# Kernel optimization log

Measured on AMD Instinct MI355X. Metric: run time of the kernel, lower is better.

The kernel has to match this reference:

```python
import jax, jax.numpy as jnp
import numpy as np
from jax import lax

B, C, H, W = 16, 128, 96, 96  # dim = C


def conv2d(x, w, b, pad, groups=1):
    y = lax.conv_general_dilated(
        x, w, window_strides=(1, 1), padding=[(pad, pad), (pad, pad)],
        dimension_numbers=("NCHW", "OIHW", "NCHW"), feature_group_count=groups)
    return y + b[None, :, None, None]


def setup_inputs() -> dict:
    key = jax.random.key(0)
    ks = jax.random.split(key, 16)
    std = 0.02
    inp = {
        "x": jax.random.normal(ks[0], (B, C, H, W), jnp.float32),
        "sin": jax.random.normal(ks[1], (H * W, C), jnp.float32),
        "cos": jax.random.normal(ks[2], (H * W, C), jnp.float32),
        # qkvo: 1x1 conv, dim -> 4*dim
        "w_qkvo": jax.random.normal(ks[3], (4 * C, C, 1, 1), jnp.float32) * std,
        "b_qkvo": jnp.zeros((4 * C,), jnp.float32),
        # lepe: 5x5 depthwise conv
        "w_lepe": jax.random.normal(ks[4], (C, 1, 5, 5), jnp.float32) * std,
        "b_lepe": jnp.zeros((C,), jnp.float32),
        # proj: 1x1 conv
        "w_proj": jax.random.normal(ks[5], (C, C, 1, 1), jnp.float32) * std,
        "b_proj": jnp.zeros((C,), jnp.float32),
        # 3x3 depthwise convs on q/k/v
        "w_q": jax.random.normal(ks[6], (C, 1, 3, 3), jnp.float32) * std,
        "b_q": jnp.zeros((C,), jnp.float32),
        "w_k": jax.random.normal(ks[7], (C, 1, 3, 3), jnp.float32) * std,
        "b_k": jnp.zeros((C,), jnp.float32),
        "w_v": jax.random.normal(ks[8], (C, 1, 3, 3), jnp.float32) * std,
        "b_v": jnp.zeros((C,), jnp.float32),
    }
    return inp


def reference(x, sin, cos, w_qkvo, b_qkvo, w_lepe, b_lepe, w_proj, b_proj,
              w_q, b_q, w_k, b_k, w_v, b_v):
    # sin/cos are accepted but unused, matching the original forward.
    b, c, h, w = x.shape
    hw = h * w
    scale = c ** (-0.5)

    qkvo = conv2d(x, w_qkvo, b_qkvo, 0)          # (B, 4C, H, W)
    qkv = qkvo[:, :3 * c]
    o = qkvo[:, 3 * c:]
    lepe = conv2d(qkv[:, 2 * c:], w_lepe, b_lepe, 2, groups=c)  # (B, C, H, W)

    q = qkv[:, :c]
    k = qkv[:, c:2 * c]
    v = qkv[:, 2 * c:]
    q = q + conv2d(q, w_q, b_q, 1, groups=c)
    k = k + conv2d(k, w_k, b_k, 1, groups=c)
    v = v + conv2d(v, w_v, b_v, 1, groups=c)

    # (B, C, H, W) -> (B, HW, C)
    to_tok = lambda t: t.reshape(b, c, hw).transpose(0, 2, 1)
    q = jax.nn.elu(to_tok(q)) + 1.0
    k = jax.nn.elu(to_tok(k)) + 1.0
    v = to_tok(v)

    k_mean = k.mean(axis=1, keepdims=True)                    # (B, 1, C)
    z = jnp.einsum("bnc,bmc->bnm", q, k_mean) * scale         # (B, HW, 1)

    s = (scale / hw) ** 0.5
    kv = jnp.einsum("bnc,bnd->bcd", k * s, v * s)             # (B, C, C)

    res = (jnp.einsum("bnc,bcd->bnd", q, kv) * (1.0 + 1.0 / (z + 1e-6))
           - z * v.mean(axis=2, keepdims=True))               # (B, HW, C)

    res = res.transpose(0, 2, 1).reshape(b, c, h, w)
    res = res + lepe
    return conv2d(res * o, w_proj, b_proj, 0)
```

## Files before the change

kernel.cpp:

```cpp
#include <hip/hip_runtime.h>
#include <math.h>

#define HW 9216
#define BSTRIDE_QKVO ((size_t)4718592)
#define BSTRIDE_C    ((size_t)1179648)
#define KVS 24

typedef __attribute__((ext_vector_type(4))) short short4v;
typedef __attribute__((ext_vector_type(8))) short short8v;
typedef __attribute__((ext_vector_type(4))) float f32x4;
typedef __attribute__((ext_vector_type(4))) unsigned short u16x4;

__device__ __forceinline__ unsigned short f2b(float f) {
  union { float f; unsigned u; } v; v.f = f;
  unsigned r = (v.u + 0x7fffu + ((v.u >> 16) & 1u)) >> 16;
  return (unsigned short)r;
}
__device__ __forceinline__ float b2f(unsigned short h) {
  union { unsigned u; float f; } v; v.u = ((unsigned)h) << 16;
  return v.f;
}

__global__ void cvt_kernel(const float* __restrict__ in, unsigned short* __restrict__ out, int n) {
  int i = blockIdx.x * 256 + threadIdx.x;
  if (i < n) out[i] = f2b(in[i]);
}

template<int BSRC_F32, int OUT_F32, int NOCB>
__global__ __launch_bounds__(256) void gemm_k128s(
    const unsigned short* __restrict__ A, const void* __restrict__ Bv,
    const float* __restrict__ bias, void* __restrict__ Ov,
    size_t bstrB, size_t bstrO)
{
  __shared__ unsigned short Bt[128 * 132];
  const int t = threadIdx.x, lane = t & 63, wave = t >> 6;
  const int wr = wave >> 1, wc = wave & 1;
  const int l4 = lane & 15, lg = lane >> 4;
  const int pb = blockIdx.x << 7, b = blockIdx.y;

  if (BSRC_F32) {
    const float* B = (const float*)Bv + (size_t)b * bstrB;
    #pragma unroll
    for (int i = 0; i < 8; ++i) {
      int id = t + (i << 8);
      int kp = id >> 5, pg = id & 31;
      const float* r0 = B + (size_t)(2 * kp) * HW + pb + (pg << 2);
      f32x4 a = *(const f32x4*)r0;
      f32x4 c = *(const f32x4*)(r0 + HW);
      #pragma unroll
      for (int j = 0; j < 4; ++j)
        *(unsigned*)&Bt[((pg << 2) + j) * 132 + 2 * kp] =
            (unsigned)f2b(a[j]) | ((unsigned)f2b(c[j]) << 16);
    }
  } else {
    const unsigned short* B = (const unsigned short*)Bv + (size_t)b * bstrB;
    #pragma unroll
    for (int i = 0; i < 8; ++i) {
      int id = t + (i << 8);
      int kp = id >> 5, pg = id & 31;
      const unsigned short* r0 = B + (size_t)(2 * kp) * HW + pb + (pg << 2);
      u16x4 a = *(const u16x4*)r0;
      u16x4 c = *(const u16x4*)(r0 + HW);
      #pragma unroll
      for (int j = 0; j < 4; ++j)
        *(unsigned*)&Bt[((pg << 2) + j) * 132 + 2 * kp] =
            (unsigned)a[j] | ((unsigned)c[j] << 16);
    }
  }

  __syncthreads();

  short8v af[4][4];
  #pragma unroll
  for (int mp = 0; mp < 4; ++mp)
    #pragma unroll
    for (int ks = 0; ks < 4; ++ks) {
      int base = (wr * 64 + mp * 16 + l4) * 132 + ks * 32 + lg * 8;
      short4v lo = *(const short4v*)&Bt[base];
      short4v hi = *(const short4v*)&Bt[base + 4];
      short8v v;
      v[0] = lo[0]; v[1] = lo[1]; v[2] = lo[2]; v[3] = lo[3];
      v[4] = hi[0]; v[5] = hi[1]; v[6] = hi[2]; v[7] = hi[3];
      af[mp][ks] = v;
    }

  for (int co = 0; co < NOCB; ++co) {
    f32x4 acc[4][4];
    #pragma unroll
    for (int mp = 0; mp < 4; ++mp)
      #pragma unroll
      for (int nd = 0; nd < 4; ++nd) acc[mp][nd] = (f32x4){0.f, 0.f, 0.f, 0.f};

    #pragma unroll
    for (int ks = 0; ks < 4; ++ks) {
      short8v bfk[4];
      #pragma unroll
      for (int nd = 0; nd < 4; ++nd)
        bfk[nd] = *(const short8v*)(A + (size_t)(co * 128 + wc * 64 + nd * 16 + l4) * 128 + ks * 32 + lg * 8);
      #pragma unroll
      for (int nd = 0; nd < 4; ++nd)
        #pragma unroll
        for (int mp = 0; mp < 4; ++mp)
          acc[mp][nd] = __builtin_amdgcn_mfma_f32_16x16x32_bf16(af[mp][ks], bfk[nd], acc[mp][nd], 0, 0, 0);
    }

    float bb[4];
    #pragma unroll
    for (int nd = 0; nd < 4; ++nd) bb[nd] = bias[co * 128 + wc * 64 + nd * 16 + l4];

    if (OUT_F32) {
      float* O = (float*)Ov + (size_t)b * bstrO;
      #pragma unroll
      for (int mp = 0; mp < 4; ++mp) {
        int px = pb + wr * 64 + mp * 16 + lg * 4;
        #pragma unroll
        for (int nd = 0; nd < 4; ++nd) {
          int oc = co * 128 + wc * 64 + nd * 16 + l4;
          f32x4 v;
          #pragma unroll
          for (int i = 0; i < 4; ++i) v[i] = acc[mp][nd][i] + bb[nd];
          *(f32x4*)&O[(size_t)oc * HW + px] = v;
        }
      }
    } else {
      unsigned short* O = (unsigned short*)Ov + (size_t)b * bstrO;
      #pragma unroll
      for (int mp = 0; mp < 4; ++mp) {
        int px = pb + wr * 64 + mp * 16 + lg * 4;
        #pragma unroll
        for (int nd = 0; nd < 4; ++nd) {
          int oc = co * 128 + wc * 64 + nd * 16 + l4;
          u16x4 v;
          #pragma unroll
          for (int i = 0; i < 4; ++i) v[i] = f2b(acc[mp][nd][i] + bb[nd]);
          *(u16x4*)&O[(size_t)oc * HW + px] = v;
        }
      }
    }
  }
}

__device__ __forceinline__ void stage_plane(const unsigned short* __restrict__ g,
                                            float* __restrict__ sp, int t) {
  #pragma unroll
  for (int i = 0; i < 9; ++i) {
    int f = (t + (i << 8)) << 2;
    u16x4 u = *(const u16x4*)&g[f];
    f32x4 fv;
    fv[0] = b2f(u[0]); fv[1] = b2f(u[1]); fv[2] = b2f(u[2]); fv[3] = b2f(u[3]);
    *(f32x4*)&sp[f] = fv;
  }
}

__device__ __forceinline__ f32x4 conv3_strip(const float* __restrict__ sp, int base,
                                             const float* __restrict__ w9,
                                             bool j0, bool j23, f32x4* cen) {
  f32x4 acc = (f32x4){0.f, 0.f, 0.f, 0.f};
  #pragma unroll
  for (int ky = 0; ky < 3; ++ky) {
    const float* rowp = sp + base + (ky - 1) * 96;
    f32x4 w0 = *(const f32x4*)(rowp - 4);
    f32x4 w1 = *(const f32x4*)(rowp);
    f32x4 w2 = *(const f32x4*)(rowp + 4);
    float xm1 = j0 ? 0.f : w0[3];
    float xp4 = j23 ? 0.f : w2[0];
    float k0 = w9[ky * 3], k1 = w9[ky * 3 + 1], k2 = w9[ky * 3 + 2];
    acc[0] += k0 * xm1   + k1 * w1[0] + k2 * w1[1];
    acc[1] += k0 * w1[0] + k1 * w1[1] + k2 * w1[2];
    acc[2] += k0 * w1[1] + k1 * w1[2] + k2 * w1[3];
    acc[3] += k0 * w1[2] + k1 * w1[3] + k2 * xp4;
    if (ky == 1) *cen = w1;
  }
  return acc;
}

__global__ __launch_bounds__(256) void dwconv_kernel(
    unsigned short* __restrict__ qkvo,
    const float* __restrict__ w_q, const float* __restrict__ b_q,
    const float* __restrict__ w_k, const float* __restrict__ b_k,
    const float* __restrict__ w_v, const float* __restrict__ b_v,
    const float* __restrict__ w_lepe, const float* __restrict__ b_lepe,
    float* __restrict__ lp, float* __restrict__ ksum)
{
  __shared__ float sb[9612];
  __shared__ float red[256];
  const int c = blockIdx.x, b = blockIdx.y, t = threadIdx.x;
  unsigned short* qg = qkvo + ((size_t)b * 512 + c) * HW;
  unsigned short* kg = qg + (size_t)128 * HW;
  unsigned short* vg = qg + (size_t)256 * HW;
  float* lg = lp + ((size_t)b * 128 + c) * HW;
  float* sp = sb + 196;

  for (int i = t; i < 384; i += 256) {
    int idx = (i < 192) ? (i - 192) : (9024 + i);
    sp[idx] = 0.f;
  }

  {
    stage_plane(qg, sp, t);
    float w9[9];
    #pragma unroll
    for (int i = 0; i < 9; ++i) w9[i] = w_q[c * 9 + i];
    float bb = b_q[c];
    __syncthreads();
    for (int i = 0; i < 9; ++i) {
      int s = t + (i << 8);
      int r = s / 24, j = s - r * 24;
      int base = r * 96 + (j << 2);
      f32x4 cen;
      f32x4 a = conv3_strip(sp, base, w9, j == 0, j == 23, &cen);
      u16x4 o;
      #pragma unroll
      for (int k = 0; k < 4; ++k) {
        float v = cen[k] + bb + a[k];
        o[k] = f2b(v > 0.f ? v + 1.f : __expf(v));
      }
      *(u16x4*)&qg[base] = o;
    }
    __syncthreads();
  }
  float kacc = 0.f;
  {
    stage_plane(kg, sp, t);
    float w9[9];
    #pragma unroll
    for (int i = 0; i < 9; ++i) w9[i] = w_k[c * 9 + i];
    float bb = b_k[c];
    __syncthreads();
    for (int i = 0; i < 9; ++i) {
      int s = t + (i << 8);
      int r = s / 24, j = s - r * 24;
      int base = r * 96 + (j << 2);
      f32x4 cen;
      f32x4 a = conv3_strip(sp, base, w9, j == 0, j == 23, &cen);
      u16x4 o;
      #pragma unroll
      for (int k = 0; k < 4; ++k) {
        float v = cen[k] + bb + a[k];
        float e = v > 0.f ? v + 1.f : __expf(v);
        o[k] = f2b(e);
        kacc += e;
      }
      *(u16x4*)&kg[base] = o;
    }
    __syncthreads();
  }
  {
    stage_plane(vg, sp, t);
    float w9[9], w25[25];
    #pragma unroll
    for (int i = 0; i < 9; ++i) w9[i] = w_v[c * 9 + i];
    #pragma unroll
    for (int i = 0; i < 25; ++i) w25[i] = w_lepe[c * 25 + i];
    float bv = b_v[c], bl = b_lepe[c];
    __syncthreads();
    for (int i = 0; i < 9; ++i) {
      int s = t + (i << 8);
      int r = s / 24, j = s - r * 24;
      int base = r * 96 + (j << 2);
      bool j0 = (j == 0), j23 = (j == 23);
      f32x4 a3 = (f32x4){0.f, 0.f, 0.f, 0.f};
      f32x4 a5 = (f32x4){0.f, 0.f, 0.f, 0.f};
      f32x4 cen = (f32x4){0.f, 0.f, 0.f, 0.f};
      #pragma unroll
      for (int ky = 0; ky < 5; ++ky) {
        const float* rowp = sp + base + (ky - 2) * 96;
        f32x4 w0 = *(const f32x4*)(rowp - 4);
        f32x4 w1 = *(const f32x4*)(rowp);
        f32x4 w2 = *(const f32x4*)(rowp + 4);
        float xm2 = j0 ? 0.f : w0[2];
        float xm1 = j0 ? 0.f : w0[3];
        float xp4 = j23 ? 0.f : w2[0];
        float xp5 = j23 ? 0.f : w2[1];
        const float* wr5 = w25 + ky * 5;
        a5[0] += wr5[0]*xm2   + wr5[1]*xm1   + wr5[2]*w1[0] + wr5[3]*w1[1] + wr5[4]*w1[2];
        a5[1] += wr5[0]*xm1   + wr5[1]*w1[0] + wr5[2]*w1[1] + wr5[3]*w1[2] + wr5[4]*w1[3];
        a5[2] += wr5[0]*w1[0] + wr5[1]*w1[1] + wr5[2]*w1[2] + wr5[3]*w1[3] + wr5[4]*xp4;
        a5[3] += wr5[0]*w1[1] + wr5[1]*w1[2] + wr5[2]*w1[3] + wr5[3]*xp4   + wr5[4]*xp5;
        if (ky >= 1 && ky <= 3) {
          float k0 = w9[(ky-1)*3], k1 = w9[(ky-1)*3+1], k2 = w9[(ky-1)*3+2];
          a3[0] += k0 * xm1   + k1 * w1[0] + k2 * w1[1];
          a3[1] += k0 * w1[0] + k1 * w1[1] + k2 * w1[2];
          a3[2] += k0 * w1[1] + k1 * w1[2] + k2 * w1[3];
          a3[3] += k0 * w1[2] + k1 * w1[3] + k2 * xp4;
          if (ky == 2) cen = w1;
        }
      }
      u16x4 o;
      f32x4 lout;
      #pragma unroll
      for (int k = 0; k < 4; ++k) {
        o[k] = f2b(cen[k] + bv + a3[k]);
        lout[k] = bl + a5[k];
      }
      *(u16x4*)&vg[base] = o;
      *(f32x4*)&lg[base] = lout;
    }
  }
  red[t] = kacc; __syncthreads();
  for (int s2 = 128; s2 > 0; s2 >>= 1) { if (t < s2) red[t] += red[t + s2]; __syncthreads(); }
  if (t == 0) ksum[b * 128 + c] = red[0];
}

__global__ __launch_bounds__(256) void kv_mfma(
    const unsigned short* __restrict__ qkvo, float* __restrict__ part)
{
  const int t = threadIdx.x, lane = t & 63, wave = t >> 6;
  const int wr = wave >> 1, wc = wave & 1;
  const int l4 = lane & 15, lg = lane >> 4;
  const int s = blockIdx.x, b = blockIdx.y;
  const unsigned short* kbase = qkvo + (size_t)b * BSTRIDE_QKVO + (size_t)128 * HW;
  const unsigned short* vbase = kbase + (size_t)128 * HW;
  const int p0 = s * 384;

  f32x4 acc[4][4];
  #pragma unroll
  for (int m = 0; m < 4; ++m)
    #pragma unroll
    for (int n = 0; n < 4; ++n) acc[m][n] = (f32x4){0.f, 0.f, 0.f, 0.f};

  for (int kk = 0; kk < 12; ++kk) {
    int p = p0 + kk * 32 + lg * 8;
    short8v ka[4], va[4];
    #pragma unroll
    for (int m = 0; m < 4; ++m) ka[m] = *(const short8v*)(kbase + (size_t)(wr * 64 + m * 16 + l4) * HW + p);
    #pragma unroll
    for (int n = 0; n < 4; ++n) va[n] = *(const short8v*)(vbase + (size_t)(wc * 64 + n * 16 + l4) * HW + p);
    #pragma unroll
    for (int n = 0; n < 4; ++n)
      #pragma unroll
      for (int m = 0; m < 4; ++m)
        acc[m][n] = __builtin_amdgcn_mfma_f32_16x16x32_bf16(ka[m], va[n], acc[m][n], 0, 0, 0);
  }

  float* pp = part + ((size_t)b * KVS + s) * 16384;
  #pragma unroll
  for (int m = 0; m < 4; ++m)
    #pragma unroll
    for (int n = 0; n < 4; ++n) {
      int d = wc * 64 + n * 16 + l4;
      #pragma unroll
      for (int i = 0; i < 4; ++i) {
        int cch = wr * 64 + m * 16 + lg * 4 + i;
        pp[(cch << 7) + d] = acc[m][n][i];
      }
    }
}

__global__ void kvreduce(const float* __restrict__ part, unsigned short* __restrict__ kvT) {
  const int b = blockIdx.y;
  const int e0 = blockIdx.x * 2048 + threadIdx.x;
  const float* pb_ = part + (size_t)b * KVS * 16384;
  for (int i = 0; i < 8; ++i) {
    int e = e0 + i * 256;
    int cch = e >> 7, d = e & 127;
    float sum = 0.f;
    #pragma unroll 8
    for (int s = 0; s < KVS; ++s) sum += pb_[(size_t)s * 16384 + e];
    kvT[(size_t)b * 16384 + d * 128 + cch] = f2b(sum);
  }
}

__global__ void vmean_k(const unsigned short* __restrict__ qkvo, float* __restrict__ vmean) {
  const int b = blockIdx.y;
  const int px = blockIdx.x * 256 + threadIdx.x;
  const unsigned short* vb = qkvo + (size_t)b * BSTRIDE_QKVO + (size_t)256 * HW + px;
  float s = 0.f;
  #pragma unroll 8
  for (int d = 0; d < 128; ++d) s += b2f(vb[(size_t)d * HW]);
  vmean[(size_t)b * HW + px] = s * (1.f / 128.f);
}

__global__ __launch_bounds__(256) void attn_mfma(
    unsigned short* __restrict__ qkvo, const unsigned short* __restrict__ kvT,
    const float* __restrict__ ksum, const float* __restrict__ vmean,
    const float* __restrict__ lp)
{
  __shared__ unsigned short Bt[128 * 132];
  __shared__ float zb[128];
  __shared__ float km[128];
  const int t = threadIdx.x, lane = t & 63, wave = t >> 6;
  const int wr = wave >> 1, wc = wave & 1;
  const int l4 = lane & 15, lg = lane >> 4;
  const int pb = blockIdx.x << 7, b = blockIdx.y;
  const float kSCf = (float)(0.08838834764831843 / 9216.0);

  unsigned short* qs = qkvo + (size_t)b * BSTRIDE_QKVO;
  const unsigned short* os = qs + (size_t)384 * HW;
  const float* lpb = lp + (size_t)b * BSTRIDE_C;

  if (t < 128) km[t] = ksum[(b << 7) + t];

  #pragma unroll
  for (int i = 0; i < 8; ++i) {
    int id = t + (i << 8);
    int kp = id >> 5, pg = id & 31;
    const unsigned short* r0 = qs + (size_t)(2 * kp) * HW + pb + (pg << 2);
    u16x4 a = *(const u16x4*)r0;
    u16x4 c = *(const u16x4*)(r0 + HW);
    #pragma unroll
    for (int j = 0; j < 4; ++j)
      *(unsigned*)&Bt[((pg << 2) + j) * 132 + 2 * kp] =
          (unsigned)a[j] | ((unsigned)c[j] << 16);
  }

  const unsigned short* Ab = kvT + (size_t)b * 16384;
  short8v bkv[4][4];
  #pragma unroll
  for (int nd = 0; nd < 4; ++nd)
    #pragma unroll
    for (int ks = 0; ks < 4; ++ks)
      bkv[nd][ks] = *(const short8v*)(Ab + (size_t)(wc * 64 + nd * 16 + l4) * 128 + ks * 32 + lg * 8);

  f32x4 acc[4][4];
  #pragma unroll
  for (int mp = 0; mp < 4; ++mp)
    #pragma unroll
    for (int nd = 0; nd < 4; ++nd) acc[mp][nd] = (f32x4){0.f, 0.f, 0.f, 0.f};

  __syncthreads();

  if (t < 128) {
    float za = 0.f;
    #pragma unroll 8
    for (int cch = 0; cch < 128; ++cch) za += b2f(Bt[t * 132 + cch]) * km[cch];
    zb[t] = za;
  }

  #pragma unroll
  for (int ks = 0; ks < 4; ++ks) {
    short8v aq[4];
    #pragma unroll
    for (int mp = 0; mp < 4; ++mp) {
      int base = (wr * 64 + mp * 16 + l4) * 132 + ks * 32 + lg * 8;
      short4v lo = *(const short4v*)&Bt[base];
      short4v hi = *(const short4v*)&Bt[base + 4];
      short8v v;
      v[0] = lo[0]; v[1] = lo[1]; v[2] = lo[2]; v[3] = lo[3];
      v[4] = hi[0]; v[5] = hi[1]; v[6] = hi[2]; v[7] = hi[3];
      aq[mp] = v;
    }
    #pragma unroll
    for (int nd = 0; nd < 4; ++nd)
      #pragma unroll
      for (int mp = 0; mp < 4; ++mp)
        acc[mp][nd] = __builtin_amdgcn_mfma_f32_16x16x32_bf16(aq[mp], bkv[nd][ks], acc[mp][nd], 0, 0, 0);
  }

  __syncthreads();

  #pragma unroll
  for (int mp = 0; mp < 4; ++mp) {
    int pxl = wr * 64 + mp * 16 + lg * 4;
    int px = pb + pxl;
    f32x4 zv = *(const f32x4*)&zb[pxl];
    f32x4 vm = *(const f32x4*)&vmean[(size_t)b * HW + px];
    f32x4 zfv, zvmv;
    #pragma unroll
    for (int i = 0; i < 4; ++i) {
      float z = zv[i] * kSCf;
      zfv[i]  = kSCf * (1.f + 1.f / (z + 1e-6f));
      zvmv[i] = z * vm[i];
    }
    #pragma unroll
    for (int nd = 0; nd < 4; ++nd) {
      int d = wc * 64 + nd * 16 + l4;
      f32x4 le = *(const f32x4*)&lpb[(size_t)d * HW + px];
      u16x4 ovv = *(const u16x4*)&os[(size_t)d * HW + px];
      u16x4 o;
      #pragma unroll
      for (int i = 0; i < 4; ++i) {
        float r = (acc[mp][nd][i] * zfv[i] - zvmv[i] + le[i]) * b2f(ovv[i]);
        o[i] = f2b(r);
      }
      *(u16x4*)&qs[(size_t)d * HW + px] = o;
    }
  }
}

extern "C" void kernel_launch(void* const* d_in, const int* in_sizes, int n_in,
                              void* d_out, int out_size, void* d_ws, size_t ws_size,
                              hipStream_t stream) {
  const float* x      = (const float*)d_in[0];
  const float* w_qkvo = (const float*)d_in[3];
  const float* b_qkvo = (const float*)d_in[4];
  const float* w_lepe = (const float*)d_in[5];
  const float* b_lepe = (const float*)d_in[6];
  const float* w_proj = (const float*)d_in[7];
  const float* b_proj = (const float*)d_in[8];
  const float* w_q = (const float*)d_in[9];
  const float* b_q = (const float*)d_in[10];
  const float* w_k = (const float*)d_in[11];
  const float* b_k = (const float*)d_in[12];
  const float* w_v = (const float*)d_in[13];
  const float* b_v = (const float*)d_in[14];
  float* out = (float*)d_out;

  unsigned short* wqh = (unsigned short*)d_ws;
  unsigned short* wph = wqh + 65536;
  const size_t perb_bytes = 9437184 + 1572864 + 32768 + 512 + 36864;
  int G = 0;
  for (int g = 16; g >= 1; g >>= 1)
    if ((size_t)163840 + (size_t)g * perb_bytes <= ws_size) { G = g; break; }
  if (G == 0) return;

  size_t off = 163840;
  unsigned short* qkvo_h = (unsigned short*)((char*)d_ws + off); off += (size_t)G * 9437184;
  float* kvpart = (float*)((char*)d_ws + off);                   off += (size_t)G * 1572864;
  unsigned short* kvT = (unsigned short*)((char*)d_ws + off);    off += (size_t)G * 32768;
  float* ksum = (float*)((char*)d_ws + off);                     off += (size_t)G * 512;
  float* vmeanp = (float*)((char*)d_ws + off);

  cvt_kernel<<<dim3(256), 256, 0, stream>>>(w_qkvo, wqh, 65536);
  cvt_kernel<<<dim3(64),  256, 0, stream>>>(w_proj, wph, 16384);

  for (int b0 = 0; b0 < 16; b0 += G) {
    const float* xc  = x   + (size_t)b0 * BSTRIDE_C;
    float*       oc_ = out + (size_t)b0 * BSTRIDE_C;

    gemm_k128s<1, 0, 4><<<dim3(72, G), 256, 0, stream>>>(
        wqh, xc, b_qkvo, qkvo_h, BSTRIDE_C, BSTRIDE_QKVO);
    dwconv_kernel<<<dim3(128, G), 256, 0, stream>>>(qkvo_h, w_q, b_q, w_k, b_k, w_v, b_v,
                                                    w_lepe, b_lepe, oc_, ksum);
    kv_mfma<<<dim3(KVS, G), 256, 0, stream>>>(qkvo_h, kvpart);
    kvreduce<<<dim3(8, G), 256, 0, stream>>>(kvpart, kvT);
    vmean_k<<<dim3(36, G), 256, 0, stream>>>(qkvo_h, vmeanp);
    attn_mfma<<<dim3(72, G), 256, 0, stream>>>(qkvo_h, kvT, ksum, vmeanp, oc_);
    gemm_k128s<0, 1, 1><<<dim3(72, G), 256, 0, stream>>>(
        wph, qkvo_h, b_proj, oc_, BSTRIDE_QKVO, BSTRIDE_C);
  }
}
```

Before: 299.4 us.

## Double-buffer GEMM input tiles across three 64-pixel tiles per block

Both 1x1-conv GEMMs now have each block handle three 64-pixel tiles instead of one 128-pixel tile. A two-slot LDS buffer lets the global loads for the next tile run while the MFMA compute for the current tile proceeds. The grid drops from 72 to 48 blocks per batch, and launch bounds now request 3 blocks per CU to keep occupancy up despite the register-held prefetch. The risks are fewer blocks for the GPU to spread across, and smaller per-wave tiles that lower MFMA reuse of the weight fragments loaded from global memory.

```diff
diff --git a/kernel.cpp b/kernel.cpp
--- a/kernel.cpp
+++ b/kernel.cpp
@@ -27,116 +27,150 @@
 }
 
 template<int BSRC_F32, int OUT_F32, int NOCB>
-__global__ __launch_bounds__(256) void gemm_k128s(
+__global__ __launch_bounds__(256, 3) void gemm_pipe(
     const unsigned short* __restrict__ A, const void* __restrict__ Bv,
     const float* __restrict__ bias, void* __restrict__ Ov,
     size_t bstrB, size_t bstrO)
 {
-  __shared__ unsigned short Bt[128 * 132];
+  __shared__ unsigned short Bt[2][64 * 132];
   const int t = threadIdx.x, lane = t & 63, wave = t >> 6;
   const int wr = wave >> 1, wc = wave & 1;
   const int l4 = lane & 15, lg = lane >> 4;
-  const int pb = blockIdx.x << 7, b = blockIdx.y;
-
-  if (BSRC_F32) {
-    const float* B = (const float*)Bv + (size_t)b * bstrB;
-    #pragma unroll
-    for (int i = 0; i < 8; ++i) {
+  const int b = blockIdx.y;
+
+  f32x4 ra[4], rc[4];
+  u16x4 ha[4], hc[4];
+
+  const float* Bf = (const float*)Bv + (size_t)b * bstrB;
+  const unsigned short* Bh = (const unsigned short*)Bv + (size_t)b * bstrB;
+
+  auto stage_load = [&](int tile) {
+    int pb = tile << 6;
+    if (BSRC_F32) {
+      #pragma unroll
+      for (int i = 0; i < 4; ++i) {
+        int id = t + (i << 8);
+        int kp = id >> 4, pg = id & 15;
+        const float* r0 = Bf + (size_t)(2 * kp) * HW + pb + (pg << 2);
+        ra[i] = *(const f32x4*)r0;
+        rc[i] = *(const f32x4*)(r0 + HW);
+      }
+    } else {
+      #pragma unroll
+      for (int i = 0; i < 4; ++i) {
+        int id = t + (i << 8);
+        int kp = id >> 4, pg = id & 15;
+        const unsigned short* r0 = Bh + (size_t)(2 * kp) * HW + pb + (pg << 2);
+        ha[i] = *(const u16x4*)r0;
+        hc[i] = *(const u16x4*)(r0 + HW);
+      }
+    }
+  };
+
+  auto stage_write = [&](int buf) {
+    unsigned short* Bb = &Bt[buf][0];
+    #pragma unroll
+    for (int i = 0; i < 4; ++i) {
       int id = t + (i << 8);
-      int kp = id >> 5, pg = id & 31;
-      const float* r0 = B + (size_t)(2 * kp) * HW + pb + (pg << 2);
-      f32x4 a = *(const f32x4*)r0;
-      f32x4 c = *(const f32x4*)(r0 + HW);
-      #pragma unroll
-      for (int j = 0; j < 4; ++j)
-        *(unsigned*)&Bt[((pg << 2) + j) * 132 + 2 * kp] =
-            (unsigned)f2b(a[j]) | ((unsigned)f2b(c[j]) << 16);
-    }
-  } else {
-    const unsigned short* B = (const unsigned short*)Bv + (size_t)b * bstrB;
-    #pragma unroll
-    for (int i = 0; i < 8; ++i) {
-      int id = t + (i << 8);
-      int kp = id >> 5, pg = id & 31;
-      const unsigned short* r0 = B + (size_t)(2 * kp) * HW + pb + (pg << 2);
-      u16x4 a = *(const u16x4*)r0;
-      u16x4 c = *(const u16x4*)(r0 + HW);
-      #pragma unroll
-      for (int j = 0; j < 4; ++j)
-        *(unsigned*)&Bt[((pg << 2) + j) * 132 + 2 * kp] =
-            (unsigned)a[j] | ((unsigned)c[j] << 16);
-    }
-  }
-
+      int kp = id >> 4, pg = id & 15;
+      if (BSRC_F32) {
+        #pragma unroll
+        for (int j = 0; j < 4; ++j)
+          *(unsigned*)&Bb[((pg << 2) + j) * 132 + 2 * kp] =
+              (unsigned)f2b(ra[i][j]) | ((unsigned)f2b(rc[i][j]) << 16);
+      } else {
+        #pragma unroll
+        for (int j = 0; j < 4; ++j)
+          *(unsigned*)&Bb[((pg << 2) + j) * 132 + 2 * kp] =
+              (unsigned)ha[i][j] | ((unsigned)hc[i][j] << 16);
+      }
+    }
+  };
+
+  auto compute_store = [&](int buf, int tile) {
+    int pb = tile << 6;
+    const unsigned short* Bb = &Bt[buf][0];
+    short8v af[2][4];
+    #pragma unroll
+    for (int mp = 0; mp < 2; ++mp)
+      #pragma unroll
+      for (int ks = 0; ks < 4; ++ks) {
+        int base = (wr * 32 + mp * 16 + l4) * 132 + ks * 32 + lg * 8;
+        short4v lo = *(const short4v*)&Bb[base];
+        short4v hi = *(const short4v*)&Bb[base + 4];
+        short8v v;
+        v[0] = lo[0]; v[1] = lo[1]; v[2] = lo[2]; v[3] = lo[3];
+        v[4] = hi[0]; v[5] = hi[1]; v[6] = hi[2]; v[7] = hi[3];
+        af[mp][ks] = v;
+      }
+
+    for (int co = 0; co < NOCB; ++co) {
+      f32x4 acc[2][4];
+      #pragma unroll
+      for (int mp = 0; mp < 2; ++mp)
+        #pragma unroll
+        for (int nd = 0; nd < 4; ++nd) acc[mp][nd] = (f32x4){0.f, 0.f, 0.f, 0.f};
+
+      #pragma unroll
+      for (int ks = 0; ks < 4; ++ks) {
+        short8v bfk[4];
+        #pragma unroll
+        for (int nd = 0; nd < 4; ++nd)
+          bfk[nd] = *(const short8v*)(A + (size_t)(co * 128 + wc * 64 + nd * 16 + l4) * 128 + ks * 32 + lg * 8);
+        #pragma unroll
+        for (int nd = 0; nd < 4; ++nd)
+          #pragma unroll
+          for (int mp = 0; mp < 2; ++mp)
+            acc[mp][nd] = __builtin_amdgcn_mfma_f32_16x16x32_bf16(af[mp][ks], bfk[nd], acc[mp][nd], 0, 0, 0);
+      }
+
+      float bb[4];
+      #pragma unroll
+      for (int nd = 0; nd < 4; ++nd) bb[nd] = bias[co * 128 + wc * 64 + nd * 16 + l4];
+
+      if (OUT_F32) {
+        float* O = (float*)Ov + (size_t)b * bstrO;
+        #pragma unroll
+        for (int mp = 0; mp < 2; ++mp) {
+          int px = pb + wr * 32 + mp * 16 + lg * 4;
+          #pragma unroll
+          for (int nd = 0; nd < 4; ++nd) {
+            int oc = co * 128 + wc * 64 + nd * 16 + l4;
+            f32x4 v;
+            #pragma unroll
+            for (int i = 0; i < 4; ++i) v[i] = acc[mp][nd][i] + bb[nd];
+            *(f32x4*)&O[(size_t)oc * HW + px] = v;
+          }
+        }
+      } else {
+        unsigned short* O = (unsigned short*)Ov + (size_t)b * bstrO;
+        #pragma unroll
+        for (int mp = 0; mp < 2; ++mp) {
+          int px = pb + wr * 32 + mp * 16 + lg * 4;
+          #pragma unroll
+          for (int nd = 0; nd < 4; ++nd) {
+            int oc = co * 128 + wc * 64 + nd * 16 + l4;
+            u16x4 v;
+            #pragma unroll
+            for (int i = 0; i < 4; ++i) v[i] = f2b(acc[mp][nd][i] + bb[nd]);
+            *(u16x4*)&O[(size_t)oc * HW + px] = v;
+          }
+        }
+      }
+    }
+  };
+
+  const int t0 = blockIdx.x * 3;
+  stage_load(t0);
+  stage_write(0);
   __syncthreads();
-
-  short8v af[4][4];
-  #pragma unroll
-  for (int mp = 0; mp < 4; ++mp)
-    #pragma unroll
-    for (int ks = 0; ks < 4; ++ks) {
-      int base = (wr * 64 + mp * 16 + l4) * 132 + ks * 32 + lg * 8;
-      short4v lo = *(const short4v*)&Bt[base];
-      short4v hi = *(const short4v*)&Bt[base + 4];
-      short8v v;
-      v[0] = lo[0]; v[1] = lo[1]; v[2] = lo[2]; v[3] = lo[3];
-      v[4] = hi[0]; v[5] = hi[1]; v[6] = hi[2]; v[7] = hi[3];
-      af[mp][ks] = v;
-    }
-
-  for (int co = 0; co < NOCB; ++co) {
-    f32x4 acc[4][4];
-    #pragma unroll
-    for (int mp = 0; mp < 4; ++mp)
-      #pragma unroll
-      for (int nd = 0; nd < 4; ++nd) acc[mp][nd] = (f32x4){0.f, 0.f, 0.f, 0.f};
-
-    #pragma unroll
-    for (int ks = 0; ks < 4; ++ks) {
-      short8v bfk[4];
-      #pragma unroll
-      for (int nd = 0; nd < 4; ++nd)
-        bfk[nd] = *(const short8v*)(A + (size_t)(co * 128 + wc * 64 + nd * 16 + l4) * 128 + ks * 32 + lg * 8);
-      #pragma unroll
-      for (int nd = 0; nd < 4; ++nd)
-        #pragma unroll
-        for (int mp = 0; mp < 4; ++mp)
-          acc[mp][nd] = __builtin_amdgcn_mfma_f32_16x16x32_bf16(af[mp][ks], bfk[nd], acc[mp][nd], 0, 0, 0);
-    }
-
-    float bb[4];
-    #pragma unroll
-    for (int nd = 0; nd < 4; ++nd) bb[nd] = bias[co * 128 + wc * 64 + nd * 16 + l4];
-
-    if (OUT_F32) {
-      float* O = (float*)Ov + (size_t)b * bstrO;
-      #pragma unroll
-      for (int mp = 0; mp < 4; ++mp) {
-        int px = pb + wr * 64 + mp * 16 + lg * 4;
-        #pragma unroll
-        for (int nd = 0; nd < 4; ++nd) {
-          int oc = co * 128 + wc * 64 + nd * 16 + l4;
-          f32x4 v;
-          #pragma unroll
-          for (int i = 0; i < 4; ++i) v[i] = acc[mp][nd][i] + bb[nd];
-          *(f32x4*)&O[(size_t)oc * HW + px] = v;
-        }
-      }
-    } else {
-      unsigned short* O = (unsigned short*)Ov + (size_t)b * bstrO;
-      #pragma unroll
-      for (int mp = 0; mp < 4; ++mp) {
-        int px = pb + wr * 64 + mp * 16 + lg * 4;
-        #pragma unroll
-        for (int nd = 0; nd < 4; ++nd) {
-          int oc = co * 128 + wc * 64 + nd * 16 + l4;
-          u16x4 v;
-          #pragma unroll
-          for (int i = 0; i < 4; ++i) v[i] = f2b(acc[mp][nd][i] + bb[nd]);
-          *(u16x4*)&O[(size_t)oc * HW + px] = v;
-        }
-      }
-    }
+  #pragma unroll
+  for (int j = 0; j < 3; ++j) {
+    int cur = j & 1;
+    if (j < 2) stage_load(t0 + j + 1);
+    compute_store(cur, t0 + j);
+    if (j < 2) stage_write(cur ^ 1);
+    __syncthreads();
   }
 }
 
@@ -518,7 +552,7 @@
     const float* xc  = x   + (size_t)b0 * BSTRIDE_C;
     float*       oc_ = out + (size_t)b0 * BSTRIDE_C;
 
-    gemm_k128s<1, 0, 4><<<dim3(72, G), 256, 0, stream>>>(
+    gemm_pipe<1, 0, 4><<<dim3(48, G), 256, 0, stream>>>(
         wqh, xc, b_qkvo, qkvo_h, BSTRIDE_C, BSTRIDE_QKVO);
     dwconv_kernel<<<dim3(128, G), 256, 0, stream>>>(qkvo_h, w_q, b_q, w_k, b_k, w_v, b_v,
                                                     w_lepe, b_lepe, oc_, ksum);
@@ -526,7 +560,7 @@
     kvreduce<<<dim3(8, G), 256, 0, stream>>>(kvpart, kvT);
     vmean_k<<<dim3(36, G), 256, 0, stream>>>(qkvo_h, vmeanp);
     attn_mfma<<<dim3(72, G), 256, 0, stream>>>(qkvo_h, kvT, ksum, vmeanp, oc_);
-    gemm_k128s<0, 1, 1><<<dim3(72, G), 256, 0, stream>>>(
+    gemm_pipe<0, 1, 1><<<dim3(48, G), 256, 0, stream>>>(
         wph, qkvo_h, b_proj, oc_, BSTRIDE_QKVO, BSTRIDE_C);
   }
 }
```

Result: slower. 318.4 us (+6.3%).

## Store lepe in bf16, fuse v-mean into kv_mfma, swizzle block order

Applied to the files above, without the earlier changes.

The lepe intermediate moves from an fp32 buffer (which was the output array) to a separate bf16 workspace buffer, halving its write and read traffic. The per-pixel mean of v is now computed inside kv_mfma from the v fragments it already loads, using lane shuffles and shared memory, so the separate vmean_k kernel and its re-read of v are removed. Block indices in the GEMM, kv and attention kernels are remapped with an XCD-style swizzle to improve cache locality across the chiplets. The trade-offs are extra bf16 rounding on lepe, additional shuffle work in kv_mfma, and a larger workspace requirement that may reduce the batch group size G.

```diff
diff --git a/kernel.cpp b/kernel.cpp
--- a/kernel.cpp
+++ b/kernel.cpp
@@ -19,6 +19,9 @@
 __device__ __forceinline__ float b2f(unsigned short h) {
   union { unsigned u; float f; } v; v.u = ((unsigned)h) << 16;
   return v.f;
+}
+__device__ __forceinline__ int xswz(int x, int nx) {
+  return (x & 7) * (nx >> 3) + (x >> 3);
 }
 
 __global__ void cvt_kernel(const float* __restrict__ in, unsigned short* __restrict__ out, int n) {
@@ -36,7 +39,7 @@
   const int t = threadIdx.x, lane = t & 63, wave = t >> 6;
   const int wr = wave >> 1, wc = wave & 1;
   const int l4 = lane & 15, lg = lane >> 4;
-  const int pb = blockIdx.x << 7, b = blockIdx.y;
+  const int pb = xswz(blockIdx.x, 72) << 7, b = blockIdx.y;
 
   if (BSRC_F32) {
     const float* B = (const float*)Bv + (size_t)b * bstrB;
@@ -180,7 +183,7 @@
     const float* __restrict__ w_k, const float* __restrict__ b_k,
     const float* __restrict__ w_v, const float* __restrict__ b_v,
     const float* __restrict__ w_lepe, const float* __restrict__ b_lepe,
-    float* __restrict__ lp, float* __restrict__ ksum)
+    unsigned short* __restrict__ lp, float* __restrict__ ksum)
 {
   __shared__ float sb[9612];
   __shared__ float red[256];
@@ -188,7 +191,7 @@
   unsigned short* qg = qkvo + ((size_t)b * 512 + c) * HW;
   unsigned short* kg = qg + (size_t)128 * HW;
   unsigned short* vg = qg + (size_t)256 * HW;
-  float* lg = lp + ((size_t)b * 128 + c) * HW;
+  unsigned short* lg = lp + ((size_t)b * 128 + c) * HW;
   float* sp = sb + 196;
 
   for (int i = t; i < 384; i += 256) {
@@ -286,15 +289,14 @@
           if (ky == 2) cen = w1;
         }
       }
-      u16x4 o;
-      f32x4 lout;
+      u16x4 o, lo16;
       #pragma unroll
       for (int k = 0; k < 4; ++k) {
         o[k] = f2b(cen[k] + bv + a3[k]);
-        lout[k] = bl + a5[k];
+        lo16[k] = f2b(bl + a5[k]);
       }
       *(u16x4*)&vg[base] = o;
-      *(f32x4*)&lg[base] = lout;
+      *(u16x4*)&lg[base] = lo16;
     }
   }
   red[t] = kacc; __syncthreads();
@@ -303,12 +305,14 @@
 }
 
 __global__ __launch_bounds__(256) void kv_mfma(
-    const unsigned short* __restrict__ qkvo, float* __restrict__ part)
+    const unsigned short* __restrict__ qkvo, float* __restrict__ part,
+    float* __restrict__ vmean)
 {
+  __shared__ float vml[2][384];
   const int t = threadIdx.x, lane = t & 63, wave = t >> 6;
   const int wr = wave >> 1, wc = wave & 1;
   const int l4 = lane & 15, lg = lane >> 4;
-  const int s = blockIdx.x, b = blockIdx.y;
+  const int s = xswz(blockIdx.x, KVS), b = blockIdx.y;
   const unsigned short* kbase = qkvo + (size_t)b * BSTRIDE_QKVO + (size_t)128 * HW;
   const unsigned short* vbase = kbase + (size_t)128 * HW;
   const int p0 = s * 384;
@@ -326,6 +330,23 @@
     for (int m = 0; m < 4; ++m) ka[m] = *(const short8v*)(kbase + (size_t)(wr * 64 + m * 16 + l4) * HW + p);
     #pragma unroll
     for (int n = 0; n < 4; ++n) va[n] = *(const short8v*)(vbase + (size_t)(wc * 64 + n * 16 + l4) * HW + p);
+
+    if (wr == 0) {
+      float pv[8];
+      #pragma unroll
+      for (int e = 0; e < 8; ++e) {
+        pv[e] = b2f((unsigned short)va[0][e]) + b2f((unsigned short)va[1][e])
+              + b2f((unsigned short)va[2][e]) + b2f((unsigned short)va[3][e]);
+        #pragma unroll
+        for (int m2 = 1; m2 < 16; m2 <<= 1)
+          pv[e] += __shfl_xor(pv[e], m2, 64);
+      }
+      if (l4 == 0) {
+        #pragma unroll
+        for (int e = 0; e < 8; ++e) vml[wc][kk * 32 + lg * 8 + e] = pv[e];
+      }
+    }
+
     #pragma unroll
     for (int n = 0; n < 4; ++n)
       #pragma unroll
@@ -345,6 +366,10 @@
         pp[(cch << 7) + d] = acc[m][n][i];
       }
     }
+
+  __syncthreads();
+  for (int i = t; i < 384; i += 256)
+    vmean[(size_t)b * HW + p0 + i] = (vml[0][i] + vml[1][i]) * (1.f / 128.f);
 }
 
 __global__ void kvreduce(const float* __restrict__ part, unsigned short* __restrict__ kvT) {
@@ -361,20 +386,10 @@
   }
 }
 
-__global__ void vmean_k(const unsigned short* __restrict__ qkvo, float* __restrict__ vmean) {
-  const int b = blockIdx.y;
-  const int px = blockIdx.x * 256 + threadIdx.x;
-  const unsigned short* vb = qkvo + (size_t)b * BSTRIDE_QKVO + (size_t)256 * HW + px;
-  float s = 0.f;
-  #pragma unroll 8
-  for (int d = 0; d < 128; ++d) s += b2f(vb[(size_t)d * HW]);
-  vmean[(size_t)b * HW + px] = s * (1.f / 128.f);
-}
-
 __global__ __launch_bounds__(256) void attn_mfma(
     unsigned short* __restrict__ qkvo, const unsigned short* __restrict__ kvT,
     const float* __restrict__ ksum, const float* __restrict__ vmean,
-    const float* __restrict__ lp)
+    const unsigned short* __restrict__ lp)
 {
   __shared__ unsigned short Bt[128 * 132];
   __shared__ float zb[128];
@@ -382,12 +397,12 @@
   const int t = threadIdx.x, lane = t & 63, wave = t >> 6;
   const int wr = wave >> 1, wc = wave & 1;
   const int l4 = lane & 15, lg = lane >> 4;
-  const int pb = blockIdx.x << 7, b = blockIdx.y;
+  const int pb = xswz(blockIdx.x, 72) << 7, b = blockIdx.y;
   const float kSCf = (float)(0.08838834764831843 / 9216.0);
 
   unsigned short* qs = qkvo + (size_t)b * BSTRIDE_QKVO;
   const unsigned short* os = qs + (size_t)384 * HW;
-  const float* lpb = lp + (size_t)b * BSTRIDE_C;
+  const unsigned short* lpb = lp + (size_t)b * BSTRIDE_C;
 
   if (t < 128) km[t] = ksum[(b << 7) + t];
 
@@ -465,12 +480,12 @@
     #pragma unroll
     for (int nd = 0; nd < 4; ++nd) {
       int d = wc * 64 + nd * 16 + l4;
-      f32x4 le = *(const f32x4*)&lpb[(size_t)d * HW + px];
+      u16x4 lev = *(const u16x4*)&lpb[(size_t)d * HW + px];
       u16x4 ovv = *(const u16x4*)&os[(size_t)d * HW + px];
       u16x4 o;
       #pragma unroll
       for (int i = 0; i < 4; ++i) {
-        float r = (acc[mp][nd][i] * zfv[i] - zvmv[i] + le[i]) * b2f(ovv[i]);
+        float r = (acc[mp][nd][i] * zfv[i] - zvmv[i] + b2f(lev[i])) * b2f(ovv[i]);
         o[i] = f2b(r);
       }
       *(u16x4*)&qs[(size_t)d * HW + px] = o;
@@ -498,7 +513,7 @@
 
   unsigned short* wqh = (unsigned short*)d_ws;
   unsigned short* wph = wqh + 65536;
-  const size_t perb_bytes = 9437184 + 1572864 + 32768 + 512 + 36864;
+  const size_t perb_bytes = 9437184 + 1572864 + 32768 + 512 + 36864 + 2359296;
   int G = 0;
   for (int g = 16; g >= 1; g >>= 1)
     if ((size_t)163840 + (size_t)g * perb_bytes <= ws_size) { G = g; break; }
@@ -509,7 +524,8 @@
   float* kvpart = (float*)((char*)d_ws + off);                   off += (size_t)G * 1572864;
   unsigned short* kvT = (unsigned short*)((char*)d_ws + off);    off += (size_t)G * 32768;
   float* ksum = (float*)((char*)d_ws + off);                     off += (size_t)G * 512;
-  float* vmeanp = (float*)((char*)d_ws + off);
+  float* vmeanp = (float*)((char*)d_ws + off);                   off += (size_t)G * 36864;
+  unsigned short* lepe_h = (unsigned short*)((char*)d_ws + off);
 
   cvt_kernel<<<dim3(256), 256, 0, stream>>>(w_qkvo, wqh, 65536);
   cvt_kernel<<<dim3(64),  256, 0, stream>>>(w_proj, wph, 16384);
@@ -521,11 +537,10 @@
     gemm_k128s<1, 0, 4><<<dim3(72, G), 256, 0, stream>>>(
         wqh, xc, b_qkvo, qkvo_h, BSTRIDE_C, BSTRIDE_QKVO);
     dwconv_kernel<<<dim3(128, G), 256, 0, stream>>>(qkvo_h, w_q, b_q, w_k, b_k, w_v, b_v,
-                                                    w_lepe, b_lepe, oc_, ksum);
-    kv_mfma<<<dim3(KVS, G), 256, 0, stream>>>(qkvo_h, kvpart);
+                                                    w_lepe, b_lepe, lepe_h, ksum);
+    kv_mfma<<<dim3(KVS, G), 256, 0, stream>>>(qkvo_h, kvpart, vmeanp);
     kvreduce<<<dim3(8, G), 256, 0, stream>>>(kvpart, kvT);
-    vmean_k<<<dim3(36, G), 256, 0, stream>>>(qkvo_h, vmeanp);
-    attn_mfma<<<dim3(72, G), 256, 0, stream>>>(qkvo_h, kvT, ksum, vmeanp, oc_);
+    attn_mfma<<<dim3(72, G), 256, 0, stream>>>(qkvo_h, kvT, ksum, vmeanp, lepe_h);
     gemm_k128s<0, 1, 1><<<dim3(72, G), 256, 0, stream>>>(
         wph, qkvo_h, b_proj, oc_, BSTRIDE_QKVO, BSTRIDE_C);
   }
```

Measured after the change: 292.8 us. 1.02x faster.
